# Kernel optimization log

Measured on AMD Instinct MI355X. Metric: run time of the kernel, lower is better.

The kernel has to match this reference:

```python
import jax, jax.numpy as jnp
import numpy as np

N = 4096      # num_nodes (tokens)
D = 1024      # in_features
GC1 = 1024    # gc hidden sizes
GC2 = 1024
FC1 = 512     # fc hidden
NUM_CLASSES = 2
FW = 8        # forward band width
BW = 8        # backward band width


def setup_inputs() -> dict:
    key = jax.random.key(0)
    ks = jax.random.split(key, 6)
    s = 0.02
    return {
        "x": jax.random.normal(ks[0], (N, D), jnp.float32),
        # sequential band weights, initialized to 0.5 as in the module
        "fw_w": 0.5 * jnp.ones((FW,), jnp.float32),
        "bw_w": 0.5 * jnp.ones((BW,), jnp.float32),
        # graph-conv layer weights (linear: h @ W + b, then A @ .)
        "gc_w1": s * jax.random.normal(ks[1], (D, GC1), jnp.float32),
        "gc_b1": jnp.zeros((GC1,), jnp.float32),
        "gc_w2": s * jax.random.normal(ks[2], (GC1, GC2), jnp.float32),
        "gc_b2": jnp.zeros((GC2,), jnp.float32),
        # fully-connected head
        "fc_w1": s * jax.random.normal(ks[3], (GC2, FC1), jnp.float32),
        "fc_b1": jnp.zeros((FC1,), jnp.float32),
        "fc_w2": s * jax.random.normal(ks[4], (FC1, NUM_CLASSES), jnp.float32),
        "fc_b2": jnp.zeros((NUM_CLASSES,), jnp.float32),
    }


def build_adjacency(fw_w, bw_w, n):
    # banded adjacency: self-loops + forward superdiagonals + backward subdiagonals,
    # then symmetric normalization D^{-1/2} A D^{-1/2}
    a = jnp.eye(n, dtype=fw_w.dtype)
    for j in range(fw_w.shape[0]):          # small fixed band loop (FW)
        a = a + fw_w[j] * jnp.eye(n, k=j + 1, dtype=fw_w.dtype)
    for j in range(bw_w.shape[0]):          # small fixed band loop (BW)
        a = a + bw_w[j] * jnp.eye(n, k=-(j + 1), dtype=bw_w.dtype)
    d = a.sum(axis=1) ** -0.5               # row degrees
    return d[:, None] * a * d[None, :]


def reference(x, fw_w, bw_w, gc_w1, gc_b1, gc_w2, gc_b2, fc_w1, fc_b1, fc_w2, fc_b2):
    a = build_adjacency(fw_w, bw_w, x.shape[0])          # [N, N]
    # GC layers: selu(A @ (H W + b)); dropout=0.0 -> identity
    h = jax.nn.selu(a @ (x @ gc_w1 + gc_b1))             # [N, GC1]
    h = jax.nn.selu(a @ (h @ gc_w2 + gc_b2))             # [N, GC2]
    pooled = h.mean(axis=0)                              # mean pooling over nodes
    z = jax.nn.selu(pooled @ fc_w1 + fc_b1)              # [FC1]
    return z @ fc_w2 + fc_b2                             # [NUM_CLASSES] logits
```

## Files before the change

kernel.cpp:

```cpp
#include <hip/hip_runtime.h>
#include <stdint.h>

#define NND 4096
#define DIM 1024
#define FC1N 512

typedef __attribute__((ext_vector_type(8))) short short8;
typedef __attribute__((ext_vector_type(4))) float floatx4;
typedef unsigned short u16;
typedef unsigned int u32;

__device__ inline u16 f2bf(float f) {
    union { float f; u32 u; } a; a.f = f;
    u32 u = a.u;
    u32 r = u + 0x7fffu + ((u >> 16) & 1u);
    return (u16)(r >> 16);
}
__device__ inline float bf2f(u16 h) {
    union { u32 u; float f; } a; a.u = ((u32)h) << 16; return a.f;
}
__device__ inline float selu_f(float x) {
    const float lam = 1.0507009873554805f;
    const float alp = 1.6732632423543772f;
    return x > 0.f ? lam * x : lam * alp * (expf(x) - 1.f);
}
__device__ inline void async16(const u16* g, u16* l) {
    __builtin_amdgcn_global_load_lds((const __attribute__((address_space(1))) u32*)g,
                                     (__attribute__((address_space(3))) u32*)l, 16, 0, 0);
}

__global__ void k_cvt_bf16(const float* __restrict__ in, u16* __restrict__ out) {
    int i = blockIdx.x * blockDim.x + threadIdx.x;
    float4 v = ((const float4*)in)[i];
    ushort4 o;
    o.x = f2bf(v.x); o.y = f2bf(v.y); o.z = f2bf(v.z); o.w = f2bf(v.w);
    ((ushort4*)out)[i] = o;
}

__global__ void k_transpose_cvt(const float* __restrict__ w1, const float* __restrict__ w2,
                                u16* __restrict__ o1, u16* __restrict__ o2) {
    const float* in = blockIdx.z ? w2 : w1;
    u16* out = blockIdx.z ? o2 : o1;
    __shared__ float tile[64][65];
    int r0 = blockIdx.x * 64;
    int c0 = blockIdx.y * 64;
    int t = threadIdx.x;
    int cg = t & 15, rb = t >> 4;
    #pragma unroll
    for (int rr = 0; rr < 4; ++rr) {
        int row = rb + rr * 16;
        float4 v = *(const float4*)(in + (size_t)(r0 + row) * DIM + c0 + cg * 4);
        tile[row][cg * 4 + 0] = v.x; tile[row][cg * 4 + 1] = v.y;
        tile[row][cg * 4 + 2] = v.z; tile[row][cg * 4 + 3] = v.w;
    }
    __syncthreads();
    #pragma unroll
    for (int rr = 0; rr < 4; ++rr) {
        int nl = rb + rr * 16;
        int kl = cg * 4;
        ushort4 o;
        o.x = f2bf(tile[kl + 0][nl]); o.y = f2bf(tile[kl + 1][nl]);
        o.z = f2bf(tile[kl + 2][nl]); o.w = f2bf(tile[kl + 3][nl]);
        *(ushort4*)(out + (size_t)(c0 + nl) * DIM + r0 + kl) = o;
    }
}

#define BM 128
#define BN 64
#define BK 64
__launch_bounds__(256)
__global__ void k_gemm_bf16(const u16* __restrict__ A, const u16* __restrict__ Bt,
                            const float* __restrict__ bias, u16* __restrict__ Y) {
    __shared__ u16 As[BM * BK];
    __shared__ u16 Bs[BN * BK];
    int m0 = blockIdx.x * BM, n0 = blockIdx.y * BN;
    int t = threadIdx.x, wave = t >> 6, lane = t & 63;
    int q = lane >> 4, r = lane & 15;
    int wm = wave & 1, wn = wave >> 1;
    int Lrow = lane >> 3, Lseg = lane & 7;
    floatx4 acc[4][2];
    #pragma unroll
    for (int mt = 0; mt < 4; ++mt) { acc[mt][0] = (floatx4)0.f; acc[mt][1] = (floatx4)0.f; }

    for (int k0 = 0; k0 < DIM; k0 += BK) {
        #pragma unroll
        for (int c = 0; c < 4; ++c) {
            int chunk = wave * 4 + c;
            int row = chunk * 8 + Lrow;
            const u16* g = A + (size_t)(m0 + row) * DIM + k0 + ((Lseg ^ (row & 7)) * 8);
            async16(g, &As[chunk * 8 * BK]);
        }
        #pragma unroll
        for (int c = 0; c < 2; ++c) {
            int chunk = wave * 2 + c;
            int row = chunk * 8 + Lrow;
            const u16* g = Bt + (size_t)(n0 + row) * DIM + k0 + ((Lseg ^ (row & 7)) * 8);
            async16(g, &Bs[chunk * 8 * BK]);
        }
        __syncthreads();
        #pragma unroll
        for (int s = 0; s < 2; ++s) {
            short8 bfrag[2];
            #pragma unroll
            for (int nt = 0; nt < 2; ++nt) {
                int n_loc = wn * 32 + nt * 16 + r;
                int phys = (s * 4 + q) ^ (n_loc & 7);
                bfrag[nt] = *(const short8*)&Bs[n_loc * BK + phys * 8];
            }
            #pragma unroll
            for (int mt = 0; mt < 4; ++mt) {
                int m_loc = wm * 64 + mt * 16 + r;
                int phys = (s * 4 + q) ^ (m_loc & 7);
                short8 afrag = *(const short8*)&As[m_loc * BK + phys * 8];
                acc[mt][0] = __builtin_amdgcn_mfma_f32_16x16x32_bf16(afrag, bfrag[0], acc[mt][0], 0, 0, 0);
                acc[mt][1] = __builtin_amdgcn_mfma_f32_16x16x32_bf16(afrag, bfrag[1], acc[mt][1], 0, 0, 0);
            }
        }
        __syncthreads();
    }
    #pragma unroll
    for (int nt = 0; nt < 2; ++nt) {
        int col = n0 + wn * 32 + nt * 16 + r;
        float bv = bias[col];
        #pragma unroll
        for (int mt = 0; mt < 4; ++mt)
            #pragma unroll
            for (int rr = 0; rr < 4; ++rr) {
                int row = m0 + wm * 64 + mt * 16 + q * 4 + rr;
                Y[(size_t)row * DIM + col] = f2bf(acc[mt][nt][rr] + bv);
            }
    }
}

__launch_bounds__(256)
__global__ void k_band(const u16* __restrict__ Y,
                       const float* __restrict__ fw, const float* __restrict__ bw,
                       u16* __restrict__ Hout, float* __restrict__ pooled, int mode) {
    __shared__ u16 tile[32][256];
    __shared__ float sdinv[32];
    __shared__ float wt[17];
    int i0 = blockIdx.x * 16;
    int c0 = blockIdx.y * 256;
    int t = threadIdx.x;
    if (t < 32) {
        int g = i0 - 8 + t;
        float deg = 1.f;
        #pragma unroll
        for (int j = 0; j < 8; ++j) {
            if (g + j + 1 < NND) deg += fw[j];
            if (g - j - 1 >= 0)  deg += bw[j];
        }
        sdinv[t] = (g >= 0 && g < NND) ? 1.f / sqrtf(deg) : 0.f;
    }
    if (t >= 32 && t < 49) {
        int o = t - 40;
        wt[t - 32] = (o == 0) ? 1.f : (o > 0 ? fw[o - 1] : bw[-o - 1]);
    }
    #pragma unroll
    for (int it = 0; it < 16; ++it) {
        int rl = it * 2 + (t >> 7);
        int g = i0 - 8 + rl;
        ushort2 v; v.x = 0; v.y = 0;
        if (g >= 0 && g < NND)
            v = *(const ushort2*)(Y + (size_t)g * DIM + c0 + (t & 127) * 2);
        *(ushort2*)&tile[rl][(t & 127) * 2] = v;
    }
    __syncthreads();
    float sv[32];
    #pragma unroll
    for (int rl = 0; rl < 32; ++rl) sv[rl] = sdinv[rl] * bf2f(tile[rl][t]);
    float psum = 0.f;
    #pragma unroll
    for (int rr = 0; rr < 16; ++rr) {
        float accv = 0.f;
        #pragma unroll
        for (int o = 0; o < 17; ++o) accv += wt[o] * sv[rr + o];
        float v = selu_f(accv * sdinv[rr + 8]);
        if (mode == 0) Hout[(size_t)(i0 + rr) * DIM + c0 + t] = f2bf(v);
        else psum += v;
    }
    if (mode == 1) atomicAdd(&pooled[c0 + t], psum);
}

__global__ void k_fc1(const float* __restrict__ pooled, const float* __restrict__ w1,
                      float* __restrict__ zacc) {
    int o = threadIdx.x;
    int kb = blockIdx.x * 64;
    float p = 0.f;
    for (int kk = 0; kk < 64; ++kk) {
        int k = kb + kk;
        p += pooled[k] * w1[(size_t)k * FC1N + o];
    }
    atomicAdd(&zacc[o], p * (1.f / NND));
}

__global__ void k_fc2(const float* __restrict__ zacc, const float* __restrict__ b1,
                      const float* __restrict__ w2, const float* __restrict__ b2,
                      float* __restrict__ out) {
    __shared__ float r0s[512], r1s[512];
    int o = threadIdx.x;
    float z = selu_f(zacc[o] + b1[o]);
    r0s[o] = z * w2[o * 2 + 0];
    r1s[o] = z * w2[o * 2 + 1];
    __syncthreads();
    for (int s = 256; s > 0; s >>= 1) {
        if (o < s) { r0s[o] += r0s[o + s]; r1s[o] += r1s[o + s]; }
        __syncthreads();
    }
    if (o == 0) { out[0] = r0s[0] + b2[0]; out[1] = r1s[0] + b2[1]; }
}

extern "C" void kernel_launch(void* const* d_in, const int* in_sizes, int n_in,
                              void* d_out, int out_size, void* d_ws, size_t ws_size,
                              hipStream_t stream) {
    const float* x     = (const float*)d_in[0];
    const float* fw    = (const float*)d_in[1];
    const float* bw    = (const float*)d_in[2];
    const float* gc_w1 = (const float*)d_in[3];
    const float* gc_b1 = (const float*)d_in[4];
    const float* gc_w2 = (const float*)d_in[5];
    const float* gc_b2 = (const float*)d_in[6];
    const float* fc_w1 = (const float*)d_in[7];
    const float* fc_b1 = (const float*)d_in[8];
    const float* fc_w2 = (const float*)d_in[9];
    const float* fc_b2 = (const float*)d_in[10];
    float* out = (float*)d_out;

    char* ws = (char*)d_ws;
    u16*   Xb     = (u16*)(ws + 0);
    u16*   W1t    = (u16*)(ws + (8u  << 20));
    u16*   W2t    = (u16*)(ws + (10u << 20));
    u16*   Yb     = (u16*)(ws + (12u << 20));
    float* pooled = (float*)(ws + (20u << 20));
    float* zacc   = (float*)(ws + (20u << 20) + 4096);

    hipMemsetAsync(pooled, 0, 4096 + 2048, stream);

    k_cvt_bf16<<<4096, 256, 0, stream>>>(x, Xb);
    k_transpose_cvt<<<dim3(16, 16, 2), 256, 0, stream>>>(gc_w1, gc_w2, W1t, W2t);

    k_gemm_bf16<<<dim3(32, 16), 256, 0, stream>>>(Xb, W1t, gc_b1, Yb);
    k_band<<<dim3(256, 4), 256, 0, stream>>>(Yb, fw, bw, Xb , nullptr, 0);
    k_gemm_bf16<<<dim3(32, 16), 256, 0, stream>>>(Xb , W2t, gc_b2, Yb);
    k_band<<<dim3(256, 4), 256, 0, stream>>>(Yb, fw, bw, nullptr, pooled, 1);
    k_fc1<<<16, 512, 0, stream>>>(pooled, fc_w1, zacc);
    k_fc2<<<1, 512, 0, stream>>>(zacc, fc_b1, fc_w2, fc_b2, out);
}
```

Baseline: 166.5 us.

## Fuse GEMM with banded adjacency epilogue, double-buffer loads, merge prep and FC kernels

Each GEMM now computes a 160-row halo tile (128 rows plus 16 above and 16 below, with recompute) and applies the banded normalized adjacency and SELU in an LDS epilogue. This removes the bf16 intermediate Y round-trip to global memory and the separate band kernels. The GEMM main loop gains double-buffered async global-to-LDS loads. The conversion, transpose and zeroing steps merge into one prep kernel, and fc1/fc2 merge via a last-block counter, cutting launches and the memset. The cost is about 25% redundant MFMA work for the halo rows and higher LDS use per block.

Result: faster. 146.7 us (-11.9%).

```diff
diff --git a/kernel.cpp b/kernel.cpp
--- a/kernel.cpp
+++ b/kernel.cpp
@@ -10,41 +10,49 @@
 typedef unsigned short u16;
 typedef unsigned int u32;
 
-__device__ inline u16 f2bf(float f) {
+__device__ __forceinline__ u16 f2bf(float f) {
     union { float f; u32 u; } a; a.f = f;
     u32 u = a.u;
-    u32 r = u + 0x7fffu + ((u >> 16) & 1u);
-    return (u16)(r >> 16);
-}
-__device__ inline float bf2f(u16 h) {
+    return (u16)((u + 0x7fffu + ((u >> 16) & 1u)) >> 16);
+}
+__device__ __forceinline__ float bf2f(u16 h) {
     union { u32 u; float f; } a; a.u = ((u32)h) << 16; return a.f;
 }
-__device__ inline float selu_f(float x) {
+__device__ __forceinline__ float selu_f(float x) {
     const float lam = 1.0507009873554805f;
     const float alp = 1.6732632423543772f;
     return x > 0.f ? lam * x : lam * alp * (expf(x) - 1.f);
 }
-__device__ inline void async16(const u16* g, u16* l) {
+__device__ __forceinline__ void async16(const u16* g, u16* l) {
     __builtin_amdgcn_global_load_lds((const __attribute__((address_space(1))) u32*)g,
                                      (__attribute__((address_space(3))) u32*)l, 16, 0, 0);
 }
 
-__global__ void k_cvt_bf16(const float* __restrict__ in, u16* __restrict__ out) {
-    int i = blockIdx.x * blockDim.x + threadIdx.x;
-    float4 v = ((const float4*)in)[i];
-    ushort4 o;
-    o.x = f2bf(v.x); o.y = f2bf(v.y); o.z = f2bf(v.z); o.w = f2bf(v.w);
-    ((ushort4*)out)[i] = o;
-}
-
-__global__ void k_transpose_cvt(const float* __restrict__ w1, const float* __restrict__ w2,
-                                u16* __restrict__ o1, u16* __restrict__ o2) {
-    const float* in = blockIdx.z ? w2 : w1;
-    u16* out = blockIdx.z ? o2 : o1;
+__global__ void k_prep(const float* __restrict__ x, const float* __restrict__ w1,
+                       const float* __restrict__ w2, u16* __restrict__ Xb,
+                       u16* __restrict__ W1t, u16* __restrict__ W2t,
+                       float* __restrict__ zero_base) {
+    int b = blockIdx.x, t = threadIdx.x;
+    if (b < 512) {
+        const float4* xin = (const float4*)x;
+        ushort4* xo = (ushort4*)Xb;
+        int base = b * 2048 + t;
+        #pragma unroll
+        for (int i = 0; i < 8; ++i) {
+            float4 v = xin[base + i * 256];
+            ushort4 o; o.x = f2bf(v.x); o.y = f2bf(v.y); o.z = f2bf(v.z); o.w = f2bf(v.w);
+            xo[base + i * 256] = o;
+        }
+        if (b == 0)
+            for (int i = t; i < 1537; i += 256) zero_base[i] = 0.f;
+        return;
+    }
+    int job = b - 512;
+    const float* in = (job & 256) ? w2 : w1;
+    u16* out = (job & 256) ? W2t : W1t;
+    int tl = job & 255;
+    int r0 = (tl >> 4) * 64, c0 = (tl & 15) * 64;
     __shared__ float tile[64][65];
-    int r0 = blockIdx.x * 64;
-    int c0 = blockIdx.y * 64;
-    int t = threadIdx.x;
     int cg = t & 15, rb = t >> 4;
     #pragma unroll
     for (int rr = 0; rr < 4; ++rr) {
@@ -65,149 +73,163 @@
     }
 }
 
-#define BM 128
-#define BN 64
-#define BK 64
-__launch_bounds__(256)
-__global__ void k_gemm_bf16(const u16* __restrict__ A, const u16* __restrict__ Bt,
-                            const float* __restrict__ bias, u16* __restrict__ Y) {
-    __shared__ u16 As[BM * BK];
-    __shared__ u16 Bs[BN * BK];
-    int m0 = blockIdx.x * BM, n0 = blockIdx.y * BN;
-    int t = threadIdx.x, wave = t >> 6, lane = t & 63;
-    int q = lane >> 4, r = lane & 15;
-    int wm = wave & 1, wn = wave >> 1;
-    int Lrow = lane >> 3, Lseg = lane & 7;
-    floatx4 acc[4][2];
-    #pragma unroll
-    for (int mt = 0; mt < 4; ++mt) { acc[mt][0] = (floatx4)0.f; acc[mt][1] = (floatx4)0.f; }
-
-    for (int k0 = 0; k0 < DIM; k0 += BK) {
-        #pragma unroll
-        for (int c = 0; c < 4; ++c) {
-            int chunk = wave * 4 + c;
-            int row = chunk * 8 + Lrow;
-            const u16* g = A + (size_t)(m0 + row) * DIM + k0 + ((Lseg ^ (row & 7)) * 8);
-            async16(g, &As[chunk * 8 * BK]);
-        }
-        #pragma unroll
-        for (int c = 0; c < 2; ++c) {
-            int chunk = wave * 2 + c;
-            int row = chunk * 8 + Lrow;
-            const u16* g = Bt + (size_t)(n0 + row) * DIM + k0 + ((Lseg ^ (row & 7)) * 8);
-            async16(g, &Bs[chunk * 8 * BK]);
-        }
+__launch_bounds__(256, 2)
+__global__ void k_gemmband(const u16* __restrict__ A, const u16* __restrict__ Bt,
+                           const float* __restrict__ bias,
+                           const float* __restrict__ fw, const float* __restrict__ bw,
+                           u16* __restrict__ H, float* __restrict__ pooled, int mode) {
+    __shared__ __align__(16) u16 stage[2][14336];
+    __shared__ float sdinv_s[160];
+    __shared__ float wt_s[17];
+    __shared__ float pl[4][64];
+
+    const int m0 = blockIdx.x * 128, n0 = blockIdx.y * 64;
+    const int t = threadIdx.x, wave = t >> 6, lane = t & 63;
+    const int q = lane >> 4, r = lane & 15;
+    const int wm = wave & 1, wn = wave >> 1;
+    const int Lrow = lane >> 3, Lseg = lane & 7;
+
+    if (t < 160) {
+        int g = m0 - 16 + t;
+        float s = 0.f;
+        if (g >= 0 && g < NND) {
+            float deg = 1.f;
+            #pragma unroll
+            for (int j = 0; j < 8; ++j) {
+                if (g + j + 1 < NND) deg += fw[j];
+                if (g - j - 1 >= 0)  deg += bw[j];
+            }
+            s = 1.f / sqrtf(deg);
+        }
+        sdinv_s[t] = s;
+    } else if (t >= 192 && t < 209) {
+        int o = t - 200;
+        wt_s[t - 192] = (o == 0) ? 1.f : (o > 0 ? fw[o - 1] : bw[-o - 1]);
+    }
+
+    floatx4 acc[5][2];
+    #pragma unroll
+    for (int mt = 0; mt < 5; ++mt) { acc[mt][0] = (floatx4)0.f; acc[mt][1] = (floatx4)0.f; }
+
+    auto issue = [&](int buf, int kb) {
+        #pragma unroll
+        for (int i = 0; i < 7; ++i) {
+            int c = wave * 7 + i;
+            u16* dst = &stage[buf][c * 512];
+            const u16* src;
+            if (c < 20) {
+                int row = c * 8 + Lrow;
+                int g = m0 - 16 + row;
+                g = g < 0 ? 0 : (g > NND - 1 ? NND - 1 : g);
+                src = A + (size_t)g * DIM + kb + ((Lseg ^ Lrow) * 8);
+            } else {
+                int row = (c - 20) * 8 + Lrow;
+                src = Bt + (size_t)(n0 + row) * DIM + kb + ((Lseg ^ Lrow) * 8);
+            }
+            async16(src, dst);
+        }
+    };
+
+    issue(0, 0);
+    #pragma unroll 1
+    for (int k = 0; k < 16; ++k) {
         __syncthreads();
+        if (k < 15) issue((k + 1) & 1, (k + 1) * 64);
+        const u16* As = &stage[k & 1][0];
+        const u16* Bs = &stage[k & 1][10240];
         #pragma unroll
         for (int s = 0; s < 2; ++s) {
-            short8 bfrag[2];
+            int j0 = s * 4 + q;
+            short8 bfr[2];
             #pragma unroll
             for (int nt = 0; nt < 2; ++nt) {
-                int n_loc = wn * 32 + nt * 16 + r;
-                int phys = (s * 4 + q) ^ (n_loc & 7);
-                bfrag[nt] = *(const short8*)&Bs[n_loc * BK + phys * 8];
-            }
-            #pragma unroll
-            for (int mt = 0; mt < 4; ++mt) {
-                int m_loc = wm * 64 + mt * 16 + r;
-                int phys = (s * 4 + q) ^ (m_loc & 7);
-                short8 afrag = *(const short8*)&As[m_loc * BK + phys * 8];
-                acc[mt][0] = __builtin_amdgcn_mfma_f32_16x16x32_bf16(afrag, bfrag[0], acc[mt][0], 0, 0, 0);
-                acc[mt][1] = __builtin_amdgcn_mfma_f32_16x16x32_bf16(afrag, bfrag[1], acc[mt][1], 0, 0, 0);
-            }
-        }
+                int nl = wn * 32 + nt * 16 + r;
+                bfr[nt] = *(const short8*)&Bs[nl * 64 + ((j0 ^ (nl & 7)) * 8)];
+            }
+            #pragma unroll
+            for (int mt = 0; mt < 5; ++mt) {
+                int ml = wm * 80 + mt * 16 + r;
+                short8 afr = *(const short8*)&As[ml * 64 + ((j0 ^ (ml & 7)) * 8)];
+                acc[mt][0] = __builtin_amdgcn_mfma_f32_16x16x32_bf16(afr, bfr[0], acc[mt][0], 0, 0, 0);
+                acc[mt][1] = __builtin_amdgcn_mfma_f32_16x16x32_bf16(afr, bfr[1], acc[mt][1], 0, 0, 0);
+            }
+        }
+    }
+    __syncthreads();
+    float (*Yt)[65] = (float(*)[65])&stage[0][0];
+    #pragma unroll
+    for (int nt = 0; nt < 2; ++nt) {
+        int col = wn * 32 + nt * 16 + r;
+        float bv = bias[n0 + col];
+        #pragma unroll
+        for (int mt = 0; mt < 5; ++mt)
+            #pragma unroll
+            for (int rr = 0; rr < 4; ++rr)
+                Yt[wm * 80 + mt * 16 + q * 4 + rr][col] = acc[mt][nt][rr] + bv;
+    }
+    __syncthreads();
+
+    int col = t & 63;
+    int r0w = (t >> 6) * 32;
+    float w[17];
+    #pragma unroll
+    for (int o = 0; o < 17; ++o) w[o] = wt_s[o];
+    float win[17];
+    #pragma unroll
+    for (int j = 0; j < 16; ++j) {
+        int T = r0w + 8 + j;
+        win[j] = sdinv_s[T] * Yt[T][col];
+    }
+    float psum = 0.f;
+    #pragma unroll
+    for (int rr = 0; rr < 32; ++rr) {
+        int T = r0w + 24 + rr;
+        win[(rr + 16) % 17] = sdinv_s[T] * Yt[T][col];
+        float a = 0.f;
+        #pragma unroll
+        for (int o = 0; o < 17; ++o) a += w[o] * win[(rr + o) % 17];
+        float v = selu_f(a * sdinv_s[r0w + 16 + rr]);
+        if (mode == 0) H[(size_t)(m0 + r0w + rr) * DIM + n0 + col] = f2bf(v);
+        else psum += v;
+    }
+    if (mode) {
+        pl[wave][col] = psum;
         __syncthreads();
-    }
-    #pragma unroll
-    for (int nt = 0; nt < 2; ++nt) {
-        int col = n0 + wn * 32 + nt * 16 + r;
-        float bv = bias[col];
-        #pragma unroll
-        for (int mt = 0; mt < 4; ++mt)
-            #pragma unroll
-            for (int rr = 0; rr < 4; ++rr) {
-                int row = m0 + wm * 64 + mt * 16 + q * 4 + rr;
-                Y[(size_t)row * DIM + col] = f2bf(acc[mt][nt][rr] + bv);
-            }
-    }
-}
-
-__launch_bounds__(256)
-__global__ void k_band(const u16* __restrict__ Y,
-                       const float* __restrict__ fw, const float* __restrict__ bw,
-                       u16* __restrict__ Hout, float* __restrict__ pooled, int mode) {
-    __shared__ u16 tile[32][256];
-    __shared__ float sdinv[32];
-    __shared__ float wt[17];
-    int i0 = blockIdx.x * 16;
-    int c0 = blockIdx.y * 256;
-    int t = threadIdx.x;
-    if (t < 32) {
-        int g = i0 - 8 + t;
-        float deg = 1.f;
-        #pragma unroll
-        for (int j = 0; j < 8; ++j) {
-            if (g + j + 1 < NND) deg += fw[j];
-            if (g - j - 1 >= 0)  deg += bw[j];
-        }
-        sdinv[t] = (g >= 0 && g < NND) ? 1.f / sqrtf(deg) : 0.f;
-    }
-    if (t >= 32 && t < 49) {
-        int o = t - 40;
-        wt[t - 32] = (o == 0) ? 1.f : (o > 0 ? fw[o - 1] : bw[-o - 1]);
-    }
-    #pragma unroll
-    for (int it = 0; it < 16; ++it) {
-        int rl = it * 2 + (t >> 7);
-        int g = i0 - 8 + rl;
-        ushort2 v; v.x = 0; v.y = 0;
-        if (g >= 0 && g < NND)
-            v = *(const ushort2*)(Y + (size_t)g * DIM + c0 + (t & 127) * 2);
-        *(ushort2*)&tile[rl][(t & 127) * 2] = v;
-    }
-    __syncthreads();
-    float sv[32];
-    #pragma unroll
-    for (int rl = 0; rl < 32; ++rl) sv[rl] = sdinv[rl] * bf2f(tile[rl][t]);
-    float psum = 0.f;
-    #pragma unroll
-    for (int rr = 0; rr < 16; ++rr) {
-        float accv = 0.f;
-        #pragma unroll
-        for (int o = 0; o < 17; ++o) accv += wt[o] * sv[rr + o];
-        float v = selu_f(accv * sdinv[rr + 8]);
-        if (mode == 0) Hout[(size_t)(i0 + rr) * DIM + c0 + t] = f2bf(v);
-        else psum += v;
-    }
-    if (mode == 1) atomicAdd(&pooled[c0 + t], psum);
-}
-
-__global__ void k_fc1(const float* __restrict__ pooled, const float* __restrict__ w1,
-                      float* __restrict__ zacc) {
-    int o = threadIdx.x;
-    int kb = blockIdx.x * 64;
-    float p = 0.f;
-    for (int kk = 0; kk < 64; ++kk) {
-        int k = kb + kk;
-        p += pooled[k] * w1[(size_t)k * FC1N + o];
-    }
-    atomicAdd(&zacc[o], p * (1.f / NND));
-}
-
-__global__ void k_fc2(const float* __restrict__ zacc, const float* __restrict__ b1,
-                      const float* __restrict__ w2, const float* __restrict__ b2,
-                      float* __restrict__ out) {
-    __shared__ float r0s[512], r1s[512];
-    int o = threadIdx.x;
-    float z = selu_f(zacc[o] + b1[o]);
-    r0s[o] = z * w2[o * 2 + 0];
-    r1s[o] = z * w2[o * 2 + 1];
-    __syncthreads();
-    for (int s = 256; s > 0; s >>= 1) {
-        if (o < s) { r0s[o] += r0s[o + s]; r1s[o] += r1s[o + s]; }
+        if (t < 64)
+            atomicAdd(&pooled[n0 + t], pl[0][t] + pl[1][t] + pl[2][t] + pl[3][t]);
+    }
+}
+
+__global__ void k_fc(const float* __restrict__ pooled, const float* __restrict__ fcw1,
+                     const float* __restrict__ fcb1, const float* __restrict__ fcw2,
+                     const float* __restrict__ fcb2, float* __restrict__ zacc,
+                     u32* __restrict__ cnt, float* __restrict__ out) {
+    __shared__ float red[1024];
+    __shared__ int lastf;
+    int o = threadIdx.x, b = blockIdx.x;
+    int kb = b * 64;
+    float s = 0.f;
+    #pragma unroll 4
+    for (int kk = 0; kk < 64; ++kk)
+        s += pooled[kb + kk] * fcw1[(size_t)(kb + kk) * FC1N + o];
+    atomicAdd(&zacc[o], s * (1.f / NND));
+    __threadfence();
+    __syncthreads();
+    if (o == 0) lastf = (atomicAdd(cnt, 1u) == 15u);
+    __syncthreads();
+    if (!lastf) return;
+    __threadfence();
+    float zv = atomicAdd(&zacc[o], 0.f);
+    float z = selu_f(zv + fcb1[o]);
+    red[o] = z * fcw2[o * 2 + 0];
+    red[512 + o] = z * fcw2[o * 2 + 1];
+    __syncthreads();
+    #pragma unroll 1
+    for (int s2 = 256; s2 > 0; s2 >>= 1) {
+        if (o < s2) { red[o] += red[o + s2]; red[512 + o] += red[512 + o + s2]; }
         __syncthreads();
     }
-    if (o == 0) { out[0] = r0s[0] + b2[0]; out[1] = r1s[0] + b2[1]; }
+    if (o == 0) { out[0] = red[0] + fcb2[0]; out[1] = red[1] + fcb2[1]; }
 }
 
 extern "C" void kernel_launch(void* const* d_in, const int* in_sizes, int n_in,
@@ -227,22 +249,16 @@
     float* out = (float*)d_out;
 
     char* ws = (char*)d_ws;
-    u16*   Xb     = (u16*)(ws + 0);
-    u16*   W1t    = (u16*)(ws + (8u  << 20));
-    u16*   W2t    = (u16*)(ws + (10u << 20));
-    u16*   Yb     = (u16*)(ws + (12u << 20));
+    u16*   Xb     = (u16*)(ws);
+    u16*   H1     = (u16*)(ws + (8u  << 20));
+    u16*   W1t    = (u16*)(ws + (16u << 20));
+    u16*   W2t    = (u16*)(ws + (18u << 20));
     float* pooled = (float*)(ws + (20u << 20));
-    float* zacc   = (float*)(ws + (20u << 20) + 4096);
-
-    hipMemsetAsync(pooled, 0, 4096 + 2048, stream);
-
-    k_cvt_bf16<<<4096, 256, 0, stream>>>(x, Xb);
-    k_transpose_cvt<<<dim3(16, 16, 2), 256, 0, stream>>>(gc_w1, gc_w2, W1t, W2t);
-
-    k_gemm_bf16<<<dim3(32, 16), 256, 0, stream>>>(Xb, W1t, gc_b1, Yb);
-    k_band<<<dim3(256, 4), 256, 0, stream>>>(Yb, fw, bw, Xb , nullptr, 0);
-    k_gemm_bf16<<<dim3(32, 16), 256, 0, stream>>>(Xb , W2t, gc_b2, Yb);
-    k_band<<<dim3(256, 4), 256, 0, stream>>>(Yb, fw, bw, nullptr, pooled, 1);
-    k_fc1<<<16, 512, 0, stream>>>(pooled, fc_w1, zacc);
-    k_fc2<<<1, 512, 0, stream>>>(zacc, fc_b1, fc_w2, fc_b2, out);
-}
+    float* zacc   = pooled + 1024;
+    u32*   cnt    = (u32*)(zacc + 512);
+
+    k_prep<<<1024, 256, 0, stream>>>(x, gc_w1, gc_w2, Xb, W1t, W2t, pooled);
+    k_gemmband<<<dim3(32, 16), 256, 0, stream>>>(Xb, W1t, gc_b1, fw, bw, H1, nullptr, 0);
+    k_gemmband<<<dim3(32, 16), 256, 0, stream>>>(H1, W2t, gc_b2, fw, bw, nullptr, pooled, 1);
+    k_fc<<<16, 512, 0, stream>>>(pooled, fc_w1, fc_b1, fc_w2, fc_b2, zacc, cnt, out);
+}
```
